# Optimization experiments

Measured on AMD Instinct MI355X. Metric: run time of the kernel, lower is better.

The kernel has to match this reference:

```python
import jax, jax.numpy as jnp
import numpy as np

B, C, LX, LY, H = 8, 128, 4096, 1024, 4
DH = C // H


def setup_inputs() -> dict:
    key = jax.random.key(0)
    ks = jax.random.split(key, 12)
    s = 0.05
    return {
        "x": jax.random.normal(ks[0], (B, C, LX), jnp.float32),
        "y": jax.random.normal(ks[1], (B, C, LY), jnp.float32),
        # nn.MultiheadAttention combined in-projection [3C, C] and bias [3C]
        "in_proj_w": jax.random.normal(ks[2], (3 * C, C), jnp.float32) * s,
        "in_proj_b": jax.random.normal(ks[3], (3 * C,), jnp.float32) * s,
        # local_att: Conv1d(C,32,1) then Conv1d(32,1,1); kernel_size=1 -> stored as matrices
        "conv1_w": jax.random.normal(ks[4], (32, C), jnp.float32) * s,
        "conv1_b": jax.random.normal(ks[5], (32,), jnp.float32) * s,
        "conv2_w": jax.random.normal(ks[6], (1, 32), jnp.float32) * s,
        "conv2_b": jax.random.normal(ks[7], (1,), jnp.float32) * s,
        # gate_mlp: Linear(2, 1)
        "gate_w": jax.random.normal(ks[8], (1, 2), jnp.float32) * s,
        "gate_b": jax.random.normal(ks[9], (1,), jnp.float32) * s,
    }


def reference(x, y, in_proj_w, in_proj_b, conv1_w, conv1_b, conv2_w, conv2_b, gate_w, gate_b):
    # x: [B,C,Lx] (query side), y: [B,C,Ly] (key/value side)
    wq, wk = in_proj_w[:C], in_proj_w[C:2 * C]
    bq, bk = in_proj_b[:C], in_proj_b[C:2 * C]

    xt = jnp.swapaxes(x, 1, 2)  # [B,Lx,C]
    yt = jnp.swapaxes(y, 1, 2)  # [B,Ly,C]

    q = (xt @ wq.T + bq).reshape(B, LX, H, DH)
    k = (yt @ wk.T + bk).reshape(B, LY, H, DH)

    scores = jnp.einsum('bqhd,bkhd->bhqk', q, k) / jnp.sqrt(jnp.float32(DH))  # [B,H,Lx,Ly]
    attn = jax.nn.softmax(scores, axis=-1)
    # torch MHA returns head-averaged weights (average_attn_weights=True)
    cross_weights = attn.mean(axis=1)            # [B,Lx,Ly]
    cross_scores = cross_weights.max(axis=-1)    # [B,Lx]
    # (attn_output / V / out_proj are unused downstream in the original forward)

    # local conv scoring (1x1 convs == channel matmuls)
    h = jax.nn.relu(jnp.einsum('oc,bcl->bol', conv1_w, x) + conv1_b[None, :, None])
    local_scores = jax.nn.sigmoid(jnp.einsum('po,bol->bpl', conv2_w, h) + conv2_b[None, :, None])[:, 0, :]  # [B,Lx]

    gating = jnp.stack((cross_scores, local_scores), axis=-1)  # [B,Lx,2]
    alpha = jax.nn.sigmoid(gating @ gate_w.T + gate_b)[..., 0]  # [B,Lx]
    return alpha * cross_scores + (1.0 - alpha) * local_scores
```

## Files before the change

kernel.cpp:

```cpp
#include <hip/hip_runtime.h>
#include <hip/hip_bf16.h>

#define BB  8
#define CC  128
#define LXX 4096
#define LYY 1024
#define HH  4
#define DHH 32

typedef __attribute__((ext_vector_type(8))) short bf16x8;
typedef __attribute__((ext_vector_type(4))) float f32x4;

static __device__ __forceinline__ unsigned short f2bf(float f) {
    __hip_bfloat16 h = __float2bfloat16(f);
    return *reinterpret_cast<unsigned short*>(&h);
}

static __device__ __forceinline__ bf16x8 pack8(const float* f) {
    bf16x8 r;
#pragma unroll
    for (int i = 0; i < 8; ++i) {
        __hip_bfloat16 h = __float2bfloat16(f[i]);
        r[i] = *reinterpret_cast<short*>(&h);
    }
    return r;
}

__global__ __launch_bounds__(256) void proj_all_kernel(
    const float* __restrict__ x, const float* __restrict__ y,
    const float* __restrict__ ipw, const float* __restrict__ ipb,
    const float* __restrict__ c1w, const float* __restrict__ c1b,
    const float* __restrict__ c2w, const float* __restrict__ c2b,
    unsigned short* __restrict__ Qb, unsigned short* __restrict__ Kb,
    float* __restrict__ localS, float qscale)
{
    int tid  = threadIdx.x;
    int wv   = tid >> 6;
    int lane = tid & 63;
    int n16  = lane & 15;
    int quad = lane >> 4;

    int blk = blockIdx.x;
    bool isX = (blk < 512);
    const float* src; const float* wrow; const float* bias;
    unsigned short* dst; int L, bi, l0; float scale;
    if (isX) {
        bi = blk >> 6; l0 = (blk & 63) * 64;
        src = x + (size_t)bi * CC * LXX; L = LXX;
        wrow = ipw; bias = ipb; dst = Qb; scale = qscale;
    } else {
        int b2 = blk - 512;
        bi = b2 >> 4; l0 = (b2 & 15) * 64;
        src = y + (size_t)bi * CC * LYY; L = LYY;
        wrow = ipw + CC * CC; bias = ipb + CC; dst = Kb; scale = 1.0f;
    }
    int lw = l0 + wv * 16;
    int myl = lw + n16;

    bf16x8 bfr[4];
#pragma unroll
    for (int kk = 0; kk < 4; ++kk) {
        float t[8];
        const float* p = src + (size_t)(kk * 32 + quad * 8) * L + myl;
#pragma unroll
        for (int j = 0; j < 8; ++j) t[j] = p[(size_t)j * L];
        bfr[kk] = pack8(t);
    }

    const f32x4 fzero = {0.f, 0.f, 0.f, 0.f};

#pragma unroll 1
    for (int m = 0; m < 8; ++m) {
        int mc = m * 16;
        f32x4 acc = fzero;
#pragma unroll
        for (int kk = 0; kk < 4; ++kk) {
            const float* wp = wrow + (size_t)(mc + n16) * CC + kk * 32 + quad * 8;
            float t[8];
            *(float4*)(t) = *(const float4*)(wp);
            *(float4*)(t + 4) = *(const float4*)(wp + 4);
            bf16x8 afr = pack8(t);
            acc = __builtin_amdgcn_mfma_f32_16x16x32_bf16(afr, bfr[kk], acc, 0, 0, 0);
        }
        int h = mc >> 5, d0 = (mc & 31) + quad * 4;
        ushort4 u;
        float4 bq = *(const float4*)(bias + mc + quad * 4);
        u.x = f2bf((acc[0] + bq.x) * scale);
        u.y = f2bf((acc[1] + bq.y) * scale);
        u.z = f2bf((acc[2] + bq.z) * scale);
        u.w = f2bf((acc[3] + bq.w) * scale);
        *(ushort4*)(dst + (((size_t)(bi * HH + h) * L) + myl) * DHH + d0) = u;
    }

    if (isX) {
        float p = 0.f;
#pragma unroll
        for (int m2 = 0; m2 < 2; ++m2) {
            f32x4 hacc = fzero;
#pragma unroll
            for (int kk = 0; kk < 4; ++kk) {
                const float* wp = c1w + (size_t)(m2 * 16 + n16) * CC + kk * 32 + quad * 8;
                float t[8];
                *(float4*)(t) = *(const float4*)(wp);
                *(float4*)(t + 4) = *(const float4*)(wp + 4);
                bf16x8 afr = pack8(t);
                hacc = __builtin_amdgcn_mfma_f32_16x16x32_bf16(afr, bfr[kk], hacc, 0, 0, 0);
            }
#pragma unroll
            for (int r = 0; r < 4; ++r) {
                int o = m2 * 16 + quad * 4 + r;
                p = fmaf(c2w[o], fmaxf(hacc[r] + c1b[o], 0.0f), p);
            }
        }
        p += __shfl_xor(p, 16, 64);
        p += __shfl_xor(p, 32, 64);
        if (quad == 0) {
            float s = p + c2b[0];
            localS[(size_t)bi * LXX + myl] = 1.0f / (1.0f + __expf(-s));
        }
    }
}

__global__ __launch_bounds__(256, 4) void attn_fused_kernel(
    const unsigned short* __restrict__ Qh, const unsigned short* __restrict__ Kh,
    const float* __restrict__ localS,
    const float* __restrict__ gw, const float* __restrict__ gb,
    float* __restrict__ out)
{
    int tid = threadIdx.x;
    int w = tid >> 6;
    int lane = tid & 63;
    int n16 = lane & 15;
    int quad = lane >> 4;
    int bi = blockIdx.y;
    int q0 = blockIdx.x * 32;

    __shared__ float dlds[4][2][HH][16];
    __shared__ float mlds[4][2][16];

    bf16x8 afr[2][HH];
#pragma unroll
    for (int qt = 0; qt < 2; ++qt)
#pragma unroll
        for (int h = 0; h < HH; ++h)
            afr[qt][h] = *(const bf16x8*)(Qh +
                (((size_t)bi * HH + h) * LXX + q0 + qt * 16 + n16) * DHH + quad * 8);

    const unsigned short* Kbase = Kh + (((size_t)bi * HH) * LYY + w * 256 + n16) * DHH + quad * 8;

    const f32x4 fzero = {0.f, 0.f, 0.f, 0.f};

    f32x4 den[2][HH];
#pragma unroll
    for (int qt = 0; qt < 2; ++qt)
#pragma unroll
        for (int h = 0; h < HH; ++h) den[qt][h] = fzero;

#pragma unroll 2
    for (int t = 0; t < 16; ++t) {
        bf16x8 bfr[HH];
#pragma unroll
        for (int h = 0; h < HH; ++h)
            bfr[h] = *(const bf16x8*)(Kbase + ((size_t)h * LYY + t * 16) * DHH);
#pragma unroll
        for (int h = 0; h < HH; ++h) {
            f32x4 s0 = __builtin_amdgcn_mfma_f32_16x16x32_bf16(afr[0][h], bfr[h], fzero, 0, 0, 0);
            f32x4 s1 = __builtin_amdgcn_mfma_f32_16x16x32_bf16(afr[1][h], bfr[h], fzero, 0, 0, 0);
#pragma unroll
            for (int r = 0; r < 4; ++r) {
                den[0][h][r] += __builtin_amdgcn_exp2f(s0[r]);
                den[1][h][r] += __builtin_amdgcn_exp2f(s1[r]);
            }
        }
    }
#pragma unroll
    for (int off = 1; off < 16; off <<= 1)
#pragma unroll
        for (int qt = 0; qt < 2; ++qt)
#pragma unroll
            for (int h = 0; h < HH; ++h)
#pragma unroll
                for (int r = 0; r < 4; ++r)
                    den[qt][h][r] += __shfl_xor(den[qt][h][r], off, 64);
    if (n16 == 0) {
#pragma unroll
        for (int qt = 0; qt < 2; ++qt)
#pragma unroll
            for (int h = 0; h < HH; ++h)
#pragma unroll
                for (int r = 0; r < 4; ++r) dlds[w][qt][h][quad * 4 + r] = den[qt][h][r];
    }
    __syncthreads();

    f32x4 cc[2][HH];
#pragma unroll
    for (int qt = 0; qt < 2; ++qt)
#pragma unroll
        for (int h = 0; h < HH; ++h)
#pragma unroll
            for (int r = 0; r < 4; ++r) {
                int row = quad * 4 + r;
                float d = dlds[0][qt][h][row] + dlds[1][qt][h][row] +
                          dlds[2][qt][h][row] + dlds[3][qt][h][row];
                cc[qt][h][r] = -__builtin_amdgcn_logf(d);
            }

    f32x4 vm0 = fzero, vm1 = fzero;
#pragma unroll 2
    for (int t = 0; t < 16; ++t) {
        bf16x8 bfr[HH];
#pragma unroll
        for (int h = 0; h < HH; ++h)
            bfr[h] = *(const bf16x8*)(Kbase + ((size_t)h * LYY + t * 16) * DHH);
        f32x4 f0 = fzero, f1 = fzero;
#pragma unroll
        for (int h = 0; h < HH; ++h) {
            f32x4 s0 = __builtin_amdgcn_mfma_f32_16x16x32_bf16(afr[0][h], bfr[h], cc[0][h], 0, 0, 0);
            f32x4 s1 = __builtin_amdgcn_mfma_f32_16x16x32_bf16(afr[1][h], bfr[h], cc[1][h], 0, 0, 0);
#pragma unroll
            for (int r = 0; r < 4; ++r) {
                f0[r] += __builtin_amdgcn_exp2f(s0[r]);
                f1[r] += __builtin_amdgcn_exp2f(s1[r]);
            }
        }
#pragma unroll
        for (int r = 0; r < 4; ++r) {
            vm0[r] = fmaxf(vm0[r], f0[r]);
            vm1[r] = fmaxf(vm1[r], f1[r]);
        }
    }
#pragma unroll
    for (int off = 1; off < 16; off <<= 1)
#pragma unroll
        for (int r = 0; r < 4; ++r) {
            vm0[r] = fmaxf(vm0[r], __shfl_xor(vm0[r], off, 64));
            vm1[r] = fmaxf(vm1[r], __shfl_xor(vm1[r], off, 64));
        }
    if (n16 == 0) {
#pragma unroll
        for (int r = 0; r < 4; ++r) {
            mlds[w][0][quad * 4 + r] = vm0[r];
            mlds[w][1][quad * 4 + r] = vm1[r];
        }
    }
    __syncthreads();
    if (tid < 32) {
        int qq = tid >> 4;
        int row = tid & 15;
        float m = fmaxf(fmaxf(mlds[0][qq][row], mlds[1][qq][row]),
                        fmaxf(mlds[2][qq][row], mlds[3][qq][row]));
        float cs = 0.25f * m;
        int orow = q0 + qq * 16 + row;
        float ls = localS[(size_t)bi * LXX + orow];
        float z = gw[0] * cs + gw[1] * ls + gb[0];
        float alpha = 1.0f / (1.0f + __expf(-z));
        out[(size_t)bi * LXX + orow] = alpha * cs + (1.0f - alpha) * ls;
    }
}

extern "C" void kernel_launch(void* const* d_in, const int* in_sizes, int n_in,
                              void* d_out, int out_size, void* d_ws, size_t ws_size,
                              hipStream_t stream) {
    const float* x   = (const float*)d_in[0];
    const float* y   = (const float*)d_in[1];
    const float* ipw = (const float*)d_in[2];
    const float* ipb = (const float*)d_in[3];
    const float* c1w = (const float*)d_in[4];
    const float* c1b = (const float*)d_in[5];
    const float* c2w = (const float*)d_in[6];
    const float* c2b = (const float*)d_in[7];
    const float* gw  = (const float*)d_in[8];
    const float* gb  = (const float*)d_in[9];
    float* out = (float*)d_out;

    float* localS = (float*)d_ws;
    unsigned short* Qb = (unsigned short*)(localS + 32768);
    unsigned short* Kb = Qb + (size_t)BB * HH * LXX * DHH;

    const float qscale = 0.17677669529663687f * 1.4426950408889634f;

    hipLaunchKernelGGL(proj_all_kernel, dim3(640), dim3(256), 0, stream,
                       x, y, ipw, ipb, c1w, c1b, c2w, c2b, Qb, Kb, localS, qscale);
    hipLaunchKernelGGL(attn_fused_kernel, dim3(LXX / 32, BB), dim3(256), 0, stream,
                       Qb, Kb, localS, gw, gb, out);
}
```

Measured before the change: 149.0 us.

## Split attention into den/max kernels over two key halves for more parallelism

Splits the single fused attention kernel into three launches. The first computes partial softmax denominators over half of the keys per block, the second recomputes scores and takes a partial max over half the keys using the combined denominators, and a small gate kernel merges the halves. This doubles the grid size (the original launched 1024 blocks) so more work is in flight, and it drops the occupancy hint from launch bounds. The cost is extra kernel launches, a global round-trip for partial results, and reloading Q in the second kernel.

```diff
diff --git a/kernel.cpp b/kernel.cpp
--- a/kernel.cpp
+++ b/kernel.cpp
@@ -121,11 +121,9 @@
     }
 }
 
-__global__ __launch_bounds__(256, 4) void attn_fused_kernel(
+__global__ __launch_bounds__(256) void attn_den_kernel(
     const unsigned short* __restrict__ Qh, const unsigned short* __restrict__ Kh,
-    const float* __restrict__ localS,
-    const float* __restrict__ gw, const float* __restrict__ gb,
-    float* __restrict__ out)
+    float* __restrict__ denp)
 {
     int tid = threadIdx.x;
     int w = tid >> 6;
@@ -134,9 +132,9 @@
     int quad = lane >> 4;
     int bi = blockIdx.y;
     int q0 = blockIdx.x * 32;
+    int half = blockIdx.z;
 
     __shared__ float dlds[4][2][HH][16];
-    __shared__ float mlds[4][2][16];
 
     bf16x8 afr[2][HH];
 #pragma unroll
@@ -146,7 +144,8 @@
             afr[qt][h] = *(const bf16x8*)(Qh +
                 (((size_t)bi * HH + h) * LXX + q0 + qt * 16 + n16) * DHH + quad * 8);
 
-    const unsigned short* Kbase = Kh + (((size_t)bi * HH) * LYY + w * 256 + n16) * DHH + quad * 8;
+    const unsigned short* Kbase = Kh +
+        (((size_t)bi * HH) * LYY + half * 512 + w * 128 + n16) * DHH + quad * 8;
 
     const f32x4 fzero = {0.f, 0.f, 0.f, 0.f};
 
@@ -157,7 +156,7 @@
         for (int h = 0; h < HH; ++h) den[qt][h] = fzero;
 
 #pragma unroll 2
-    for (int t = 0; t < 16; ++t) {
+    for (int t = 0; t < 8; ++t) {
         bf16x8 bfr[HH];
 #pragma unroll
         for (int h = 0; h < HH; ++h)
@@ -192,6 +191,40 @@
     }
     __syncthreads();
 
+    if (tid < 128) {
+        int qt  = tid >> 6;
+        int h   = (tid >> 4) & 3;
+        int row = tid & 15;
+        float d = (dlds[0][qt][h][row] + dlds[1][qt][h][row]) +
+                  (dlds[2][qt][h][row] + dlds[3][qt][h][row]);
+        denp[(((size_t)half * BB + bi) * HH + h) * LXX + q0 + qt * 16 + row] = d;
+    }
+}
+
+__global__ __launch_bounds__(256) void attn_max_kernel(
+    const unsigned short* __restrict__ Qh, const unsigned short* __restrict__ Kh,
+    const float* __restrict__ denp,
+    float* __restrict__ maxp)
+{
+    int tid = threadIdx.x;
+    int w = tid >> 6;
+    int lane = tid & 63;
+    int n16 = lane & 15;
+    int quad = lane >> 4;
+    int bi = blockIdx.y;
+    int q0 = blockIdx.x * 32;
+    int half = blockIdx.z;
+
+    __shared__ float mlds[4][2][16];
+
+    bf16x8 afr[2][HH];
+#pragma unroll
+    for (int qt = 0; qt < 2; ++qt)
+#pragma unroll
+        for (int h = 0; h < HH; ++h)
+            afr[qt][h] = *(const bf16x8*)(Qh +
+                (((size_t)bi * HH + h) * LXX + q0 + qt * 16 + n16) * DHH + quad * 8);
+
     f32x4 cc[2][HH];
 #pragma unroll
     for (int qt = 0; qt < 2; ++qt)
@@ -199,15 +232,20 @@
         for (int h = 0; h < HH; ++h)
 #pragma unroll
             for (int r = 0; r < 4; ++r) {
-                int row = quad * 4 + r;
-                float d = dlds[0][qt][h][row] + dlds[1][qt][h][row] +
-                          dlds[2][qt][h][row] + dlds[3][qt][h][row];
+                int row = q0 + qt * 16 + quad * 4 + r;
+                float d = denp[(((size_t)0 * BB + bi) * HH + h) * LXX + row] +
+                          denp[(((size_t)1 * BB + bi) * HH + h) * LXX + row];
                 cc[qt][h][r] = -__builtin_amdgcn_logf(d);
             }
+
+    const unsigned short* Kbase = Kh +
+        (((size_t)bi * HH) * LYY + half * 512 + w * 128 + n16) * DHH + quad * 8;
+
+    const f32x4 fzero = {0.f, 0.f, 0.f, 0.f};
 
     f32x4 vm0 = fzero, vm1 = fzero;
 #pragma unroll 2
-    for (int t = 0; t < 16; ++t) {
+    for (int t = 0; t < 8; ++t) {
         bf16x8 bfr[HH];
 #pragma unroll
         for (int h = 0; h < HH; ++h)
@@ -249,13 +287,22 @@
         int row = tid & 15;
         float m = fmaxf(fmaxf(mlds[0][qq][row], mlds[1][qq][row]),
                         fmaxf(mlds[2][qq][row], mlds[3][qq][row]));
-        float cs = 0.25f * m;
-        int orow = q0 + qq * 16 + row;
-        float ls = localS[(size_t)bi * LXX + orow];
-        float z = gw[0] * cs + gw[1] * ls + gb[0];
-        float alpha = 1.0f / (1.0f + __expf(-z));
-        out[(size_t)bi * LXX + orow] = alpha * cs + (1.0f - alpha) * ls;
-    }
+        maxp[((size_t)half * BB + bi) * LXX + q0 + qq * 16 + row] = m;
+    }
+}
+
+__global__ __launch_bounds__(256) void gate_kernel(
+    const float* __restrict__ maxp, const float* __restrict__ localS,
+    const float* __restrict__ gw, const float* __restrict__ gb,
+    float* __restrict__ out)
+{
+    int i = blockIdx.x * 256 + threadIdx.x;
+    float m = fmaxf(maxp[i], maxp[(size_t)BB * LXX + i]);
+    float cs = 0.25f * m;
+    float ls = localS[i];
+    float z = gw[0] * cs + gw[1] * ls + gb[0];
+    float alpha = 1.0f / (1.0f + __expf(-z));
+    out[i] = alpha * cs + (1.0f - alpha) * ls;
 }
 
 extern "C" void kernel_launch(void* const* d_in, const int* in_sizes, int n_in,
@@ -276,11 +323,17 @@
     float* localS = (float*)d_ws;
     unsigned short* Qb = (unsigned short*)(localS + 32768);
     unsigned short* Kb = Qb + (size_t)BB * HH * LXX * DHH;
+    float* denp = (float*)(Kb + (size_t)BB * HH * LYY * DHH);
+    float* maxp = denp + (size_t)2 * BB * HH * LXX;
 
     const float qscale = 0.17677669529663687f * 1.4426950408889634f;
 
     hipLaunchKernelGGL(proj_all_kernel, dim3(640), dim3(256), 0, stream,
                        x, y, ipw, ipb, c1w, c1b, c2w, c2b, Qb, Kb, localS, qscale);
-    hipLaunchKernelGGL(attn_fused_kernel, dim3(LXX / 32, BB), dim3(256), 0, stream,
-                       Qb, Kb, localS, gw, gb, out);
-}
+    hipLaunchKernelGGL(attn_den_kernel, dim3(LXX / 32, BB, 2), dim3(256), 0, stream,
+                       Qb, Kb, denp);
+    hipLaunchKernelGGL(attn_max_kernel, dim3(LXX / 32, BB, 2), dim3(256), 0, stream,
+                       Qb, Kb, denp, maxp);
+    hipLaunchKernelGGL(gate_kernel, dim3(BB * LXX / 256), dim3(256), 0, stream,
+                       maxp, localS, gw, gb, out);
+}
```

Measured after the change: 162.8 us. 1.09x slower.

## Fuse Q projection and local conv scoring into attention kernel via LDS

Applied to the files above, without the earlier changes.

Q projection and the local conv scoring move from the projection kernel into the attention kernel. Each block projects its 32 query rows from x into LDS, and computes the local scores into shared memory. This removes the global round trip for the Q buffer and localS and shrinks the first kernel to K projection only, so the second kernel can start sooner. The cost is extra per-block prologue work (strided x loads plus MFMAs) and extra LDS use in the attention kernel, which may affect occupancy.

```diff
diff --git a/kernel.cpp b/kernel.cpp
--- a/kernel.cpp
+++ b/kernel.cpp
@@ -26,13 +26,16 @@
     return r;
 }
 
-__global__ __launch_bounds__(256) void proj_all_kernel(
-    const float* __restrict__ x, const float* __restrict__ y,
-    const float* __restrict__ ipw, const float* __restrict__ ipb,
-    const float* __restrict__ c1w, const float* __restrict__ c1b,
-    const float* __restrict__ c2w, const float* __restrict__ c2b,
-    unsigned short* __restrict__ Qb, unsigned short* __restrict__ Kb,
-    float* __restrict__ localS, float qscale)
+static __device__ __forceinline__ bf16x8 ldw8(const float* p) {
+    float t[8];
+    *(float4*)(t)     = *(const float4*)(p);
+    *(float4*)(t + 4) = *(const float4*)(p + 4);
+    return pack8(t);
+}
+
+__global__ __launch_bounds__(256) void kproj_kernel(
+    const float* __restrict__ y, const float* __restrict__ ipw,
+    const float* __restrict__ ipb, unsigned short* __restrict__ Kb)
 {
     int tid  = threadIdx.x;
     int wv   = tid >> 6;
@@ -41,91 +44,50 @@
     int quad = lane >> 4;
 
     int blk = blockIdx.x;
-    bool isX = (blk < 512);
-    const float* src; const float* wrow; const float* bias;
-    unsigned short* dst; int L, bi, l0; float scale;
-    if (isX) {
-        bi = blk >> 6; l0 = (blk & 63) * 64;
-        src = x + (size_t)bi * CC * LXX; L = LXX;
-        wrow = ipw; bias = ipb; dst = Qb; scale = qscale;
-    } else {
-        int b2 = blk - 512;
-        bi = b2 >> 4; l0 = (b2 & 15) * 64;
-        src = y + (size_t)bi * CC * LYY; L = LYY;
-        wrow = ipw + CC * CC; bias = ipb + CC; dst = Kb; scale = 1.0f;
-    }
-    int lw = l0 + wv * 16;
-    int myl = lw + n16;
+    int bi = blk >> 4, l0 = (blk & 15) * 64;
+    const float* src  = y + (size_t)bi * CC * LYY;
+    const float* wrow = ipw + CC * CC;
+    const float* bias = ipb + CC;
+    int myl = l0 + wv * 16 + n16;
 
     bf16x8 bfr[4];
 #pragma unroll
     for (int kk = 0; kk < 4; ++kk) {
         float t[8];
-        const float* p = src + (size_t)(kk * 32 + quad * 8) * L + myl;
-#pragma unroll
-        for (int j = 0; j < 8; ++j) t[j] = p[(size_t)j * L];
+        const float* p = src + (size_t)(kk * 32 + quad * 8) * LYY + myl;
+#pragma unroll
+        for (int j = 0; j < 8; ++j) t[j] = p[(size_t)j * LYY];
         bfr[kk] = pack8(t);
     }
 
     const f32x4 fzero = {0.f, 0.f, 0.f, 0.f};
-
 #pragma unroll 1
     for (int m = 0; m < 8; ++m) {
         int mc = m * 16;
         f32x4 acc = fzero;
 #pragma unroll
-        for (int kk = 0; kk < 4; ++kk) {
-            const float* wp = wrow + (size_t)(mc + n16) * CC + kk * 32 + quad * 8;
-            float t[8];
-            *(float4*)(t) = *(const float4*)(wp);
-            *(float4*)(t + 4) = *(const float4*)(wp + 4);
-            bf16x8 afr = pack8(t);
-            acc = __builtin_amdgcn_mfma_f32_16x16x32_bf16(afr, bfr[kk], acc, 0, 0, 0);
-        }
+        for (int kk = 0; kk < 4; ++kk)
+            acc = __builtin_amdgcn_mfma_f32_16x16x32_bf16(
+                ldw8(wrow + (size_t)(mc + n16) * CC + kk * 32 + quad * 8),
+                bfr[kk], acc, 0, 0, 0);
         int h = mc >> 5, d0 = (mc & 31) + quad * 4;
+        float4 bq = *(const float4*)(bias + mc + quad * 4);
         ushort4 u;
-        float4 bq = *(const float4*)(bias + mc + quad * 4);
-        u.x = f2bf((acc[0] + bq.x) * scale);
-        u.y = f2bf((acc[1] + bq.y) * scale);
-        u.z = f2bf((acc[2] + bq.z) * scale);
-        u.w = f2bf((acc[3] + bq.w) * scale);
-        *(ushort4*)(dst + (((size_t)(bi * HH + h) * L) + myl) * DHH + d0) = u;
-    }
-
-    if (isX) {
-        float p = 0.f;
-#pragma unroll
-        for (int m2 = 0; m2 < 2; ++m2) {
-            f32x4 hacc = fzero;
-#pragma unroll
-            for (int kk = 0; kk < 4; ++kk) {
-                const float* wp = c1w + (size_t)(m2 * 16 + n16) * CC + kk * 32 + quad * 8;
-                float t[8];
-                *(float4*)(t) = *(const float4*)(wp);
-                *(float4*)(t + 4) = *(const float4*)(wp + 4);
-                bf16x8 afr = pack8(t);
-                hacc = __builtin_amdgcn_mfma_f32_16x16x32_bf16(afr, bfr[kk], hacc, 0, 0, 0);
-            }
-#pragma unroll
-            for (int r = 0; r < 4; ++r) {
-                int o = m2 * 16 + quad * 4 + r;
-                p = fmaf(c2w[o], fmaxf(hacc[r] + c1b[o], 0.0f), p);
-            }
-        }
-        p += __shfl_xor(p, 16, 64);
-        p += __shfl_xor(p, 32, 64);
-        if (quad == 0) {
-            float s = p + c2b[0];
-            localS[(size_t)bi * LXX + myl] = 1.0f / (1.0f + __expf(-s));
-        }
+        u.x = f2bf(acc[0] + bq.x);
+        u.y = f2bf(acc[1] + bq.y);
+        u.z = f2bf(acc[2] + bq.z);
+        u.w = f2bf(acc[3] + bq.w);
+        *(ushort4*)(Kb + (((size_t)(bi * HH + h) * LYY) + myl) * DHH + d0) = u;
     }
 }
 
 __global__ __launch_bounds__(256, 4) void attn_fused_kernel(
-    const unsigned short* __restrict__ Qh, const unsigned short* __restrict__ Kh,
-    const float* __restrict__ localS,
+    const float* __restrict__ x, const unsigned short* __restrict__ Kh,
+    const float* __restrict__ ipw, const float* __restrict__ ipb,
+    const float* __restrict__ c1w, const float* __restrict__ c1b,
+    const float* __restrict__ c2w, const float* __restrict__ c2b,
     const float* __restrict__ gw, const float* __restrict__ gb,
-    float* __restrict__ out)
+    float* __restrict__ out, float qscale)
 {
     int tid = threadIdx.x;
     int w = tid >> 6;
@@ -135,20 +97,74 @@
     int bi = blockIdx.y;
     int q0 = blockIdx.x * 32;
 
+    __shared__ unsigned short qlds[2][16][136];
     __shared__ float dlds[4][2][HH][16];
     __shared__ float mlds[4][2][16];
+    __shared__ float plds[32];
+
+    const float* xsrc = x + (size_t)bi * CC * LXX;
+    const f32x4 fzero = {0.f, 0.f, 0.f, 0.f};
+
+#pragma unroll 1
+    for (int qt = 0; qt < 2; ++qt) {
+        bf16x8 bq[4];
+#pragma unroll
+        for (int kk = 0; kk < 4; ++kk) {
+            float t[8];
+            const float* p = xsrc + (size_t)(kk * 32 + quad * 8) * LXX + q0 + qt * 16 + n16;
+#pragma unroll
+            for (int j = 0; j < 8; ++j) t[j] = p[(size_t)j * LXX];
+            bq[kk] = pack8(t);
+        }
+#pragma unroll
+        for (int mi = 0; mi < 2; ++mi) {
+            int m = 2 * w + mi;
+            f32x4 acc = fzero;
+#pragma unroll
+            for (int kk = 0; kk < 4; ++kk)
+                acc = __builtin_amdgcn_mfma_f32_16x16x32_bf16(
+                    ldw8(ipw + (size_t)(m * 16 + n16) * CC + kk * 32 + quad * 8),
+                    bq[kk], acc, 0, 0, 0);
+            float4 bv = *(const float4*)(ipb + m * 16 + quad * 4);
+            ushort4 u;
+            u.x = f2bf((acc[0] + bv.x) * qscale);
+            u.y = f2bf((acc[1] + bv.y) * qscale);
+            u.z = f2bf((acc[2] + bv.z) * qscale);
+            u.w = f2bf((acc[3] + bv.w) * qscale);
+            *(ushort4*)(&qlds[qt][n16][m * 16 + quad * 4]) = u;
+        }
+        if (w == 2 + qt) {
+            float p = 0.f;
+#pragma unroll
+            for (int m2 = 0; m2 < 2; ++m2) {
+                f32x4 hacc = fzero;
+#pragma unroll
+                for (int kk = 0; kk < 4; ++kk)
+                    hacc = __builtin_amdgcn_mfma_f32_16x16x32_bf16(
+                        ldw8(c1w + (size_t)(m2 * 16 + n16) * CC + kk * 32 + quad * 8),
+                        bq[kk], hacc, 0, 0, 0);
+#pragma unroll
+                for (int r = 0; r < 4; ++r) {
+                    int o = m2 * 16 + quad * 4 + r;
+                    p = fmaf(c2w[o], fmaxf(hacc[r] + c1b[o], 0.0f), p);
+                }
+            }
+            p += __shfl_xor(p, 16, 64);
+            p += __shfl_xor(p, 32, 64);
+            if (quad == 0)
+                plds[qt * 16 + n16] = 1.0f / (1.0f + __expf(-(p + c2b[0])));
+        }
+    }
+    __syncthreads();
 
     bf16x8 afr[2][HH];
 #pragma unroll
     for (int qt = 0; qt < 2; ++qt)
 #pragma unroll
         for (int h = 0; h < HH; ++h)
-            afr[qt][h] = *(const bf16x8*)(Qh +
-                (((size_t)bi * HH + h) * LXX + q0 + qt * 16 + n16) * DHH + quad * 8);
+            afr[qt][h] = *(const bf16x8*)(&qlds[qt][n16][h * 32 + quad * 8]);
 
     const unsigned short* Kbase = Kh + (((size_t)bi * HH) * LYY + w * 256 + n16) * DHH + quad * 8;
-
-    const f32x4 fzero = {0.f, 0.f, 0.f, 0.f};
 
     f32x4 den[2][HH];
 #pragma unroll
@@ -251,7 +267,7 @@
                         fmaxf(mlds[2][qq][row], mlds[3][qq][row]));
         float cs = 0.25f * m;
         int orow = q0 + qq * 16 + row;
-        float ls = localS[(size_t)bi * LXX + orow];
+        float ls = plds[qq * 16 + row];
         float z = gw[0] * cs + gw[1] * ls + gb[0];
         float alpha = 1.0f / (1.0f + __expf(-z));
         out[(size_t)bi * LXX + orow] = alpha * cs + (1.0f - alpha) * ls;
@@ -273,14 +289,12 @@
     const float* gb  = (const float*)d_in[9];
     float* out = (float*)d_out;
 
-    float* localS = (float*)d_ws;
-    unsigned short* Qb = (unsigned short*)(localS + 32768);
-    unsigned short* Kb = Qb + (size_t)BB * HH * LXX * DHH;
+    unsigned short* Kb = (unsigned short*)d_ws;
 
     const float qscale = 0.17677669529663687f * 1.4426950408889634f;
 
-    hipLaunchKernelGGL(proj_all_kernel, dim3(640), dim3(256), 0, stream,
-                       x, y, ipw, ipb, c1w, c1b, c2w, c2b, Qb, Kb, localS, qscale);
+    hipLaunchKernelGGL(kproj_kernel, dim3(128), dim3(256), 0, stream,
+                       y, ipw, ipb, Kb);
     hipLaunchKernelGGL(attn_fused_kernel, dim3(LXX / 32, BB), dim3(256), 0, stream,
-                       Qb, Kb, localS, gw, gb, out);
-}
+                       x, Kb, ipw, ipb, c1w, c1b, c2w, c2b, gw, gb, out, qscale);
+}
```

After: 139.5 us. -6.3%, faster.
